# Kernel optimization log

Hardware: AMD Instinct MI355X
Metric: run time of the kernel (lower is better)

Reference implementation:

```python
import jax, jax.numpy as jnp
import numpy as np

N = 20000      # nodes
E = 320000     # edges (avg degree 16)
HID = 128      # hidden_channel
OUT = 128      # output_channel
SEQ = 8


def setup_inputs() -> dict:
    key = jax.random.key(0)
    ks = jax.random.split(key, 8)
    h = jax.random.normal(ks[0], (N, HID), jnp.float32)
    c = jax.random.normal(ks[1], (N, HID), jnp.float32)
    edge_index = jax.random.randint(ks[2], (2, E), 0, N, jnp.int64)
    edge_attr = jax.random.uniform(ks[3], (E,), jnp.float32)
    # GCNConv weights (PyG: x @ W then propagate), xavier-ish scale
    W_init = jax.random.normal(ks[4], (2 * HID, 2 * OUT), jnp.float32) * (2.0 / (2 * HID + 2 * OUT)) ** 0.5
    b_init = jnp.zeros((2 * OUT,), jnp.float32)
    W_cell = jax.random.normal(ks[5], (HID + OUT, 4 * OUT), jnp.float32) * (2.0 / (HID + OUT + 4 * OUT)) ** 0.5
    b_cell = jnp.zeros((4 * OUT,), jnp.float32)
    return {"h": h, "c": c, "edge_index": edge_index, "edge_attr": edge_attr,
            "W_init": W_init, "b_init": b_init, "W_cell": W_cell, "b_cell": b_cell,
            "seq_len": SEQ}


def _gcn(x, W, b, src, dst, ew, dinv):
    # PyG GCNConv with normalize=True, add_self_loops=True (self-loop weight 1.0)
    xw = x @ W                                   # [N, C_out]
    norm = dinv[src] * ew * dinv[dst]            # sym-normalized edge weights
    agg = jnp.zeros_like(xw).at[dst].add(xw[src] * norm[:, None])
    agg = agg + xw * (dinv * dinv)[:, None]      # self-loop term
    return agg + b


def reference(h, c, edge_index, edge_attr, W_init, b_init, W_cell, b_cell, seq_len):
    src, dst = edge_index[0], edge_index[1]
    n = h.shape[0]
    # degree with self-loops (weight 1.0), shared by both convs
    deg = jnp.zeros((n,), h.dtype).at[dst].add(edge_attr) + 1.0
    dinv = jax.lax.rsqrt(deg)

    # _init_states
    states = jax.nn.elu(_gcn(jnp.concatenate([h, c], axis=1), W_init, b_init, src, dst, edge_attr, dinv))
    h_t, c_t = states[:, :OUT], states[:, OUT:]

    def step(carry, _):
        h_cur, c_cur = carry
        # NOTE: original code feeds the initial h (not h_cur) as x each step
        combined = jnp.concatenate([h, h_cur], axis=1)
        cc = _gcn(combined, W_cell, b_cell, src, dst, edge_attr, dinv)
        cc_i, cc_f, cc_o, cc_g = jnp.split(cc, 4, axis=1)
        c_next = jax.nn.sigmoid(cc_f) * c_cur + jax.nn.sigmoid(cc_i) * jnp.tanh(cc_g)
        h_next = jax.nn.sigmoid(cc_o) * jnp.tanh(c_next)
        return (h_next, c_next), h_next

    (_, _), out = jax.lax.scan(step, (h_t, c_t), None, length=seq_len)
    return out  # [seq_len, N, OUT]
```

## Files before the change

### kernel.cpp

```cpp
#include <hip/hip_runtime.h>

#define N_NODES 20000
#define N_EDGES 320000
#define SEQ 8

typedef __attribute__((ext_vector_type(8))) short bf16x8;
typedef __attribute__((ext_vector_type(4))) float floatx4;
typedef const unsigned int __attribute__((address_space(1)))* gas_u32;
typedef unsigned int __attribute__((address_space(3)))* las_u32;

__device__ __forceinline__ unsigned short f2bf(float f) {
  unsigned int u = __builtin_bit_cast(unsigned int, f);
  return (unsigned short)((u + 0x7fffu + ((u >> 16) & 1u)) >> 16);
}
__device__ __forceinline__ float bflo(unsigned int u) {
  return __builtin_bit_cast(float, u << 16);
}
__device__ __forceinline__ float bfhi(unsigned int u) {
  return __builtin_bit_cast(float, u & 0xffff0000u);
}
__device__ __forceinline__ float sigf(float x) { return 1.f / (1.f + __expf(-x)); }

__device__ __forceinline__ void gl_lds16(const void* g, void* l) {
  auto gp = (gas_u32)g;
  auto lp = (las_u32)(unsigned int)(unsigned long long)l;
  __builtin_amdgcn_global_load_lds(gp, lp, 16, 0, 0);
}


__global__ void k_prologue(const float* __restrict__ Wi,
                           const float* __restrict__ Wc,
                           const float* __restrict__ bc,
                           unsigned short* __restrict__ WiT,
                           unsigned short* __restrict__ W1T,
                           unsigned short* __restrict__ W2T,
                           float* __restrict__ bcp,
                           float* __restrict__ deg, int* __restrict__ counts) {
  int idx = blockIdx.x * 256 + threadIdx.x;
  if (idx < N_NODES) { deg[idx] = 1.0f; counts[idx] = 0; }
  if (idx < 65536) {
    int n = idx >> 8, k = idx & 255;
    WiT[n * 256 + k] = f2bf(Wi[k * 256 + n]);
  }
  if (idx < 512) bcp[idx] = bc[((idx & 3) << 7) | (idx >> 2)];
  int n2 = idx >> 8, k2 = idx & 255;
  if (k2 < 128) {
    int orig = ((n2 & 3) << 7) | (n2 >> 2);
    W1T[n2 * 128 + k2] = f2bf(Wc[k2 * 512 + orig]);
    W2T[n2 * 128 + k2] = f2bf(Wc[(k2 + 128) * 512 + orig]);
  }
}

__global__ void k_deg(const int* __restrict__ ei, const float* __restrict__ ea,
                      float* __restrict__ deg, int* __restrict__ counts) {
  int e = blockIdx.x * 256 + threadIdx.x;
  if (e >= N_EDGES) return;
  int d = ei[N_EDGES + e];
  atomicAdd(&deg[d], ea[e]);
  atomicAdd(&counts[d], 1);
}

__global__ void k_scan1(const int* __restrict__ counts, int* __restrict__ incl,
                        int* __restrict__ part, const float* __restrict__ deg,
                        float* __restrict__ dinv) {
  __shared__ int sm[256];
  int t = threadIdx.x;
  int g = blockIdx.x * 256 + t;
  if (g < N_NODES) dinv[g] = rsqrtf(deg[g]);
  int v = (g < N_NODES) ? counts[g] : 0;
  sm[t] = v;
  __syncthreads();
  for (int o = 1; o < 256; o <<= 1) {
    int add = (t >= o) ? sm[t - o] : 0;
    __syncthreads();
    sm[t] += add;
    __syncthreads();
  }
  if (g < N_NODES) incl[g] = sm[t];
  if (t == 255) part[blockIdx.x] = sm[255];
}

__global__ void k_scan2(int* __restrict__ part, int nb) {
  __shared__ int sm[128];
  int t = threadIdx.x;
  int v = (t < nb) ? part[t] : 0;
  sm[t] = v;
  __syncthreads();
  for (int o = 1; o < 128; o <<= 1) {
    int add = (t >= o) ? sm[t - o] : 0;
    __syncthreads();
    sm[t] += add;
    __syncthreads();
  }
  if (t < nb) part[t] = sm[t] - v;
}

__global__ void k_scan3(const int* __restrict__ incl, const int* __restrict__ counts,
                        const int* __restrict__ part, int* __restrict__ row_ptr,
                        int* __restrict__ cursor) {
  int g = blockIdx.x * 256 + threadIdx.x;
  if (g < N_NODES) {
    int start = incl[g] - counts[g] + part[blockIdx.x];
    row_ptr[g] = start;
    cursor[g] = start;
  }
  if (g == 0) row_ptr[N_NODES] = N_EDGES;
}

__global__ void k_fill(const int* __restrict__ ei, const float* __restrict__ ea,
                       const float* __restrict__ dinv, int* __restrict__ cursor,
                       int* __restrict__ csr_src, float* __restrict__ csr_w) {
  int e = blockIdx.x * 256 + threadIdx.x;
  if (e >= N_EDGES) return;
  int s = ei[e], d = ei[N_EDGES + e];
  int k = atomicAdd(&cursor[d], 1);
  csr_src[k] = s;
  csr_w[k] = dinv[s] * ea[e] * dinv[d];
}


__global__ __launch_bounds__(256) void k_agg_init(
    const float* __restrict__ h, const float* __restrict__ c,
    unsigned int* __restrict__ AhAc_u, const float* __restrict__ dinv,
    const int* __restrict__ row_ptr, const int* __restrict__ csr_src,
    const float* __restrict__ csr_w) {
  int wid = (blockIdx.x * 256 + threadIdx.x) >> 6;
  int lane = threadIdx.x & 63;
  if (wid >= N_NODES) return;
  float di = dinv[wid], dd = di * di;
  const float4* xb = (lane < 32) ? (const float4*)h : (const float4*)c;
  int lcol = lane & 31;
  float4 a = xb[(size_t)wid * 32 + lcol];
  float s0 = a.x * dd, s1 = a.y * dd, s2 = a.z * dd, s3 = a.w * dd;
  int e = row_ptr[wid], end = row_ptr[wid + 1];
#pragma unroll 2
  for (; e < end; ++e) {
    int s = csr_src[e];
    float w = csr_w[e];
    float4 v = xb[(size_t)s * 32 + lcol];
    s0 += v.x * w; s1 += v.y * w; s2 += v.z * w; s3 += v.w * w;
  }
  uint2 o;
  o.x = (unsigned int)f2bf(s0) | ((unsigned int)f2bf(s1) << 16);
  o.y = (unsigned int)f2bf(s2) | ((unsigned int)f2bf(s3) << 16);
  ((uint2*)AhAc_u)[(size_t)wid * 64 + lane] = o;
}

__global__ __launch_bounds__(256) void k_agg_step(
    const unsigned int* __restrict__ hbf_u, unsigned int* __restrict__ Aht_u,
    const float* __restrict__ dinv, const int* __restrict__ row_ptr,
    const int* __restrict__ csr_src, const float* __restrict__ csr_w) {
  int wid = (blockIdx.x * 256 + threadIdx.x) >> 6;
  int lane = threadIdx.x & 63;
  if (wid >= N_NODES) return;
  float di = dinv[wid], dd = di * di;
  unsigned int a = hbf_u[(size_t)wid * 64 + lane];
  float s0 = bflo(a) * dd, s1 = bfhi(a) * dd;
  int e = row_ptr[wid], end = row_ptr[wid + 1];
#pragma unroll 2
  for (; e < end; ++e) {
    int s = csr_src[e];
    float w = csr_w[e];
    unsigned int v = hbf_u[(size_t)s * 64 + lane];
    s0 += bflo(v) * w;
    s1 += bfhi(v) * w;
  }
  Aht_u[(size_t)wid * 64 + lane] =
      (unsigned int)f2bf(s0) | ((unsigned int)f2bf(s1) << 16);
}

template <int EPI, int KK, int LDA>
__global__ __launch_bounds__(256) void k_gemm(
    const unsigned short* __restrict__ A, const unsigned short* __restrict__ BT,
    const float* __restrict__ bias, const float* __restrict__ Kbuf,
    float* __restrict__ c_cur, unsigned short* __restrict__ hbf,
    float* __restrict__ out0) {
  __shared__ __align__(16) union {
    struct { unsigned short a[128 * 64]; unsigned short b[128 * 64]; } ab;
    float ep[64 * 132];
  } sm;
  const int M = N_NODES;
  int tid = threadIdx.x;
  int bm0 = blockIdx.x * 128, bn0 = blockIdx.y * 128;
  int wave = tid >> 6, lane = tid & 63;
  int wrow = (wave >> 1) * 64, wcol = (wave & 1) * 64;
  int lr = lane & 15, lq = lane >> 4;
  int key = lr & 7;

  int lr8 = lane >> 3, cq = lane & 7;
  int gq8 = (cq ^ lr8) * 8;

  floatx4 acc[4][4];
#pragma unroll
  for (int i = 0; i < 4; i++)
#pragma unroll
    for (int j = 0; j < 4; j++) acc[i][j] = (floatx4){0.f, 0.f, 0.f, 0.f};

  for (int k0 = 0; k0 < KK; k0 += 64) {
    __syncthreads();
#pragma unroll
    for (int p = 0; p < 4; ++p) {
      int row = p * 32 + wave * 8;
      int ra = bm0 + row + lr8;
      if (ra > M - 1) ra = M - 1;
      gl_lds16(A + (size_t)ra * LDA + k0 + gq8, sm.ab.a + row * 64);
      gl_lds16(BT + (size_t)(bn0 + row + lr8) * KK + k0 + gq8,
               sm.ab.b + row * 64);
    }
    __syncthreads();
#pragma unroll
    for (int ks = 0; ks < 2; ++ks) {
      int q = ks * 4 + lq;
      int slot = (q ^ key) << 3;
      bf16x8 af[4], bfr[4];
#pragma unroll
      for (int mi = 0; mi < 4; mi++)
        af[mi] = *(const bf16x8*)(sm.ab.a + (wrow + mi * 16 + lr) * 64 + slot);
#pragma unroll
      for (int ni = 0; ni < 4; ni++)
        bfr[ni] = *(const bf16x8*)(sm.ab.b + (wcol + ni * 16 + lr) * 64 + slot);
#pragma unroll
      for (int mi = 0; mi < 4; mi++)
#pragma unroll
        for (int ni = 0; ni < 4; ni++)
          acc[mi][ni] = __builtin_amdgcn_mfma_f32_16x16x32_bf16(
              af[mi], bfr[ni], acc[mi][ni], 0, 0, 0);
    }
  }
  __syncthreads();

  if (EPI == 0) {
#pragma unroll
    for (int mi = 0; mi < 4; mi++) {
#pragma unroll
      for (int r = 0; r < 4; r++) {
        int grow = bm0 + wrow + mi * 16 + lq * 4 + r;
        if (grow >= M) continue;
#pragma unroll
        for (int ni = 0; ni < 4; ni++) {
          int gcol = bn0 + wcol + ni * 16 + lr;
          float v = acc[mi][ni][r] + bias[gcol];
          v = (v > 0.f) ? v : expm1f(v);
          if (gcol < 128) hbf[(size_t)grow * 128 + gcol] = f2bf(v);
          else c_cur[(size_t)grow * 128 + gcol - 128] = v;
        }
      }
    }
  } else if (EPI == 1) {
#pragma unroll
    for (int mi = 0; mi < 4; mi++) {
#pragma unroll
      for (int r = 0; r < 4; r++) {
        int grow = bm0 + wrow + mi * 16 + lq * 4 + r;
        if (grow >= M) continue;
#pragma unroll
        for (int ni = 0; ni < 4; ni++) {
          int gcol = bn0 + wcol + ni * 16 + lr;
          out0[(size_t)grow * 512 + gcol] = acc[mi][ni][r] + bias[gcol];
        }
      }
    }
  } else {
#pragma unroll
    for (int hch = 0; hch < 2; ++hch) {
      if ((wrow >> 6) == hch) {
#pragma unroll
        for (int mi = 0; mi < 4; mi++)
#pragma unroll
          for (int r = 0; r < 4; r++) {
            int row_l = mi * 16 + lq * 4 + r;
#pragma unroll
            for (int ni = 0; ni < 4; ni++)
              sm.ep[row_l * 132 + wcol + ni * 16 + lr] = acc[mi][ni][r];
          }
      }
      __syncthreads();
#pragma unroll
      for (int it = 0; it < 8; ++it) {
        int p = tid + it * 256;
        int row_l = p >> 5, j = p & 31;
        int grow = bm0 + hch * 64 + row_l;
        if (grow < M) {
          int jg = (bn0 >> 2) + j;
          const float* eb = sm.ep + row_l * 132 + 4 * j;
          float4 kb = *(const float4*)&Kbuf[(size_t)grow * 512 + bn0 + 4 * j];
          float gi = eb[0] + kb.x;
          float gf = eb[1] + kb.y;
          float go = eb[2] + kb.z;
          float gg = eb[3] + kb.w;
          size_t o = (size_t)grow * 128 + jg;
          float cp = c_cur[o];
          float cn = sigf(gf) * cp + sigf(gi) * tanhf(gg);
          float hn = sigf(go) * tanhf(cn);
          c_cur[o] = cn;
          hbf[o] = f2bf(hn);
          out0[o] = hn;
        }
      }
      __syncthreads();
    }
  }
}

extern "C" void kernel_launch(void* const* d_in, const int* in_sizes, int n_in,
                              void* d_out, int out_size, void* d_ws, size_t ws_size,
                              hipStream_t stream) {
  const float* h  = (const float*)d_in[0];
  const float* c  = (const float*)d_in[1];
  const int*   ei = (const int*)d_in[2];
  const float* ea = (const float*)d_in[3];
  const float* Wi = (const float*)d_in[4];
  const float* bi = (const float*)d_in[5];
  const float* Wc = (const float*)d_in[6];
  const float* bc = (const float*)d_in[7];
  float* out = (float*)d_out;

  char* w = (char*)d_ws;
  size_t off = 0;
  auto alloc = [&](size_t bytes) {
    void* p = w + off;
    off += (bytes + 511) & ~(size_t)511;
    return p;
  };
  float* deg           = (float*)alloc(N_NODES * 4);
  float* dinv          = (float*)alloc(N_NODES * 4);
  int* counts          = (int*)alloc(N_NODES * 4);
  int* cursor          = (int*)alloc(N_NODES * 4);
  int* scan_tmp        = (int*)alloc(N_NODES * 4);
  int* row_ptr         = (int*)alloc((N_NODES + 1) * 4);
  int* part            = (int*)alloc(1024 * 4);
  int* csr_src         = (int*)alloc(N_EDGES * 4);
  float* csr_w         = (float*)alloc(N_EDGES * 4);
  unsigned short* WiT  = (unsigned short*)alloc(256 * 256 * 2);
  unsigned short* W1T  = (unsigned short*)alloc(512 * 128 * 2);
  unsigned short* W2T  = (unsigned short*)alloc(512 * 128 * 2);
  float* bcp           = (float*)alloc(512 * 4);
  unsigned short* AhAc = (unsigned short*)alloc((size_t)N_NODES * 256 * 2);
  unsigned short* Aht  = (unsigned short*)alloc((size_t)N_NODES * 128 * 2);
  unsigned short* hbf  = (unsigned short*)alloc((size_t)N_NODES * 128 * 2);
  float* c_cur         = (float*)alloc((size_t)N_NODES * 128 * 4);
  float* Kbuf          = (float*)alloc((size_t)N_NODES * 512 * 4);

  const int NB_N = (N_NODES + 255) / 256;
  const int NB_E = (N_EDGES + 255) / 256;
  const int NB_AGG = N_NODES * 64 / 256;
  const int MB = (N_NODES + 127) / 128;

  k_prologue<<<512, 256, 0, stream>>>(Wi, Wc, bc, WiT, W1T, W2T, bcp, deg,
                                      counts);
  k_deg<<<NB_E, 256, 0, stream>>>(ei, ea, deg, counts);
  k_scan1<<<NB_N, 256, 0, stream>>>(counts, scan_tmp, part, deg, dinv);
  k_scan2<<<1, 128, 0, stream>>>(part, NB_N);
  k_scan3<<<NB_N, 256, 0, stream>>>(scan_tmp, counts, part, row_ptr, cursor);
  k_fill<<<NB_E, 256, 0, stream>>>(ei, ea, dinv, cursor, csr_src, csr_w);

  k_agg_init<<<NB_AGG, 256, 0, stream>>>(h, c, (unsigned int*)AhAc, dinv,
                                         row_ptr, csr_src, csr_w);
  k_gemm<0, 256, 256><<<dim3(MB, 2), 256, 0, stream>>>(
      AhAc, WiT, bi, nullptr, c_cur, hbf, nullptr);
  k_gemm<1, 128, 256><<<dim3(MB, 4), 256, 0, stream>>>(
      AhAc, W1T, bcp, nullptr, nullptr, nullptr, Kbuf);

  for (int t = 0; t < SEQ; ++t) {
    k_agg_step<<<NB_AGG, 256, 0, stream>>>((unsigned int*)hbf,
                                           (unsigned int*)Aht, dinv, row_ptr,
                                           csr_src, csr_w);
    k_gemm<2, 128, 128><<<dim3(MB, 4), 256, 0, stream>>>(
        Aht, W2T, nullptr, Kbuf, c_cur, hbf, out + (size_t)t * N_NODES * 128);
  }
}
```

Before: 567.0 us.

## Merge three-kernel prefix scan into one block and batch CSR index loads via shuffles

Replaces the three-kernel scan (block scan, partial scan, fixup) with a single 1024-thread block kernel where each thread serially scans 20 counts, removing two launches and the temporary buffers. In both aggregation kernels, each wavefront now loads up to 64 edge indices and weights cooperatively in one coalesced load and broadcasts them with shuffles, issuing four neighbor-row gathers per iteration. This aims to cut scalar-dependent latency in the edge loop and raise memory-level parallelism. The single-block scan has strided, uncoalesced accesses, and the shuffles add some per-edge cost.

New measurement: 534.7 us. 5.7% less time.

```diff
diff --git a/kernel.cpp b/kernel.cpp
--- a/kernel.cpp
+++ b/kernel.cpp
@@ -60,51 +60,42 @@
   atomicAdd(&counts[d], 1);
 }
 
-__global__ void k_scan1(const int* __restrict__ counts, int* __restrict__ incl,
-                        int* __restrict__ part, const float* __restrict__ deg,
-                        float* __restrict__ dinv) {
-  __shared__ int sm[256];
+__global__ __launch_bounds__(1024) void k_scan(
+    const int* __restrict__ counts, const float* __restrict__ deg,
+    float* __restrict__ dinv, int* __restrict__ row_ptr,
+    int* __restrict__ cursor) {
+  __shared__ int sm[1024];
   int t = threadIdx.x;
-  int g = blockIdx.x * 256 + t;
-  if (g < N_NODES) dinv[g] = rsqrtf(deg[g]);
-  int v = (g < N_NODES) ? counts[g] : 0;
-  sm[t] = v;
+  int base = t * 20;
+  int local[20];
+  int s = 0;
+#pragma unroll
+  for (int i = 0; i < 20; ++i) {
+    int g = base + i;
+    int v = (g < N_NODES) ? counts[g] : 0;
+    local[i] = v;
+    s += v;
+  }
+  sm[t] = s;
   __syncthreads();
-  for (int o = 1; o < 256; o <<= 1) {
+  for (int o = 1; o < 1024; o <<= 1) {
     int add = (t >= o) ? sm[t - o] : 0;
     __syncthreads();
     sm[t] += add;
     __syncthreads();
   }
-  if (g < N_NODES) incl[g] = sm[t];
-  if (t == 255) part[blockIdx.x] = sm[255];
-}
-
-__global__ void k_scan2(int* __restrict__ part, int nb) {
-  __shared__ int sm[128];
-  int t = threadIdx.x;
-  int v = (t < nb) ? part[t] : 0;
-  sm[t] = v;
-  __syncthreads();
-  for (int o = 1; o < 128; o <<= 1) {
-    int add = (t >= o) ? sm[t - o] : 0;
-    __syncthreads();
-    sm[t] += add;
-    __syncthreads();
-  }
-  if (t < nb) part[t] = sm[t] - v;
-}
-
-__global__ void k_scan3(const int* __restrict__ incl, const int* __restrict__ counts,
-                        const int* __restrict__ part, int* __restrict__ row_ptr,
-                        int* __restrict__ cursor) {
-  int g = blockIdx.x * 256 + threadIdx.x;
-  if (g < N_NODES) {
-    int start = incl[g] - counts[g] + part[blockIdx.x];
-    row_ptr[g] = start;
-    cursor[g] = start;
-  }
-  if (g == 0) row_ptr[N_NODES] = N_EDGES;
+  int run = sm[t] - s;
+#pragma unroll
+  for (int i = 0; i < 20; ++i) {
+    int g = base + i;
+    if (g < N_NODES) {
+      row_ptr[g] = run;
+      cursor[g] = run;
+      dinv[g] = rsqrtf(deg[g]);
+    }
+    run += local[i];
+  }
+  if (t == 0) row_ptr[N_NODES] = N_EDGES;
 }
 
 __global__ void k_fill(const int* __restrict__ ei, const float* __restrict__ ea,
@@ -132,13 +123,37 @@
   int lcol = lane & 31;
   float4 a = xb[(size_t)wid * 32 + lcol];
   float s0 = a.x * dd, s1 = a.y * dd, s2 = a.z * dd, s3 = a.w * dd;
-  int e = row_ptr[wid], end = row_ptr[wid + 1];
-#pragma unroll 2
-  for (; e < end; ++e) {
-    int s = csr_src[e];
-    float w = csr_w[e];
-    float4 v = xb[(size_t)s * 32 + lcol];
-    s0 += v.x * w; s1 += v.y * w; s2 += v.z * w; s3 += v.w * w;
+  int e0 = row_ptr[wid], end = row_ptr[wid + 1];
+  for (int base = e0; base < end; base += 64) {
+    int n = end - base;
+    if (n > 64) n = 64;
+    int sl = 0;
+    float wl = 0.f;
+    if (base + lane < end) {
+      sl = csr_src[base + lane];
+      wl = csr_w[base + lane];
+    }
+    int j = 0;
+    for (; j + 4 <= n; j += 4) {
+      int sa = __shfl(sl, j), sb = __shfl(sl, j + 1);
+      int sc = __shfl(sl, j + 2), sd = __shfl(sl, j + 3);
+      float wa = __shfl(wl, j), wb = __shfl(wl, j + 1);
+      float wc = __shfl(wl, j + 2), wd = __shfl(wl, j + 3);
+      float4 va = xb[(size_t)sa * 32 + lcol];
+      float4 vb = xb[(size_t)sb * 32 + lcol];
+      float4 vc = xb[(size_t)sc * 32 + lcol];
+      float4 vd = xb[(size_t)sd * 32 + lcol];
+      s0 += va.x * wa; s1 += va.y * wa; s2 += va.z * wa; s3 += va.w * wa;
+      s0 += vb.x * wb; s1 += vb.y * wb; s2 += vb.z * wb; s3 += vb.w * wb;
+      s0 += vc.x * wc; s1 += vc.y * wc; s2 += vc.z * wc; s3 += vc.w * wc;
+      s0 += vd.x * wd; s1 += vd.y * wd; s2 += vd.z * wd; s3 += vd.w * wd;
+    }
+    for (; j < n; ++j) {
+      int sa = __shfl(sl, j);
+      float wa = __shfl(wl, j);
+      float4 va = xb[(size_t)sa * 32 + lcol];
+      s0 += va.x * wa; s1 += va.y * wa; s2 += va.z * wa; s3 += va.w * wa;
+    }
   }
   uint2 o;
   o.x = (unsigned int)f2bf(s0) | ((unsigned int)f2bf(s1) << 16);
@@ -156,14 +171,37 @@
   float di = dinv[wid], dd = di * di;
   unsigned int a = hbf_u[(size_t)wid * 64 + lane];
   float s0 = bflo(a) * dd, s1 = bfhi(a) * dd;
-  int e = row_ptr[wid], end = row_ptr[wid + 1];
-#pragma unroll 2
-  for (; e < end; ++e) {
-    int s = csr_src[e];
-    float w = csr_w[e];
-    unsigned int v = hbf_u[(size_t)s * 64 + lane];
-    s0 += bflo(v) * w;
-    s1 += bfhi(v) * w;
+  int e0 = row_ptr[wid], end = row_ptr[wid + 1];
+  for (int base = e0; base < end; base += 64) {
+    int n = end - base;
+    if (n > 64) n = 64;
+    int sl = 0;
+    float wl = 0.f;
+    if (base + lane < end) {
+      sl = csr_src[base + lane];
+      wl = csr_w[base + lane];
+    }
+    int j = 0;
+    for (; j + 4 <= n; j += 4) {
+      int sa = __shfl(sl, j), sb = __shfl(sl, j + 1);
+      int sc = __shfl(sl, j + 2), sd = __shfl(sl, j + 3);
+      float wa = __shfl(wl, j), wb = __shfl(wl, j + 1);
+      float wc = __shfl(wl, j + 2), wd = __shfl(wl, j + 3);
+      unsigned int va = hbf_u[(size_t)sa * 64 + lane];
+      unsigned int vb = hbf_u[(size_t)sb * 64 + lane];
+      unsigned int vc = hbf_u[(size_t)sc * 64 + lane];
+      unsigned int vd = hbf_u[(size_t)sd * 64 + lane];
+      s0 += bflo(va) * wa; s1 += bfhi(va) * wa;
+      s0 += bflo(vb) * wb; s1 += bfhi(vb) * wb;
+      s0 += bflo(vc) * wc; s1 += bfhi(vc) * wc;
+      s0 += bflo(vd) * wd; s1 += bfhi(vd) * wd;
+    }
+    for (; j < n; ++j) {
+      int sa = __shfl(sl, j);
+      float wa = __shfl(wl, j);
+      unsigned int va = hbf_u[(size_t)sa * 64 + lane];
+      s0 += bflo(va) * wa; s1 += bfhi(va) * wa;
+    }
   }
   Aht_u[(size_t)wid * 64 + lane] =
       (unsigned int)f2bf(s0) | ((unsigned int)f2bf(s1) << 16);
@@ -326,9 +364,7 @@
   float* dinv          = (float*)alloc(N_NODES * 4);
   int* counts          = (int*)alloc(N_NODES * 4);
   int* cursor          = (int*)alloc(N_NODES * 4);
-  int* scan_tmp        = (int*)alloc(N_NODES * 4);
   int* row_ptr         = (int*)alloc((N_NODES + 1) * 4);
-  int* part            = (int*)alloc(1024 * 4);
   int* csr_src         = (int*)alloc(N_EDGES * 4);
   float* csr_w         = (float*)alloc(N_EDGES * 4);
   unsigned short* WiT  = (unsigned short*)alloc(256 * 256 * 2);
@@ -341,7 +377,6 @@
   float* c_cur         = (float*)alloc((size_t)N_NODES * 128 * 4);
   float* Kbuf          = (float*)alloc((size_t)N_NODES * 512 * 4);
 
-  const int NB_N = (N_NODES + 255) / 256;
   const int NB_E = (N_EDGES + 255) / 256;
   const int NB_AGG = N_NODES * 64 / 256;
   const int MB = (N_NODES + 127) / 128;
@@ -349,9 +384,7 @@
   k_prologue<<<512, 256, 0, stream>>>(Wi, Wc, bc, WiT, W1T, W2T, bcp, deg,
                                       counts);
   k_deg<<<NB_E, 256, 0, stream>>>(ei, ea, deg, counts);
-  k_scan1<<<NB_N, 256, 0, stream>>>(counts, scan_tmp, part, deg, dinv);
-  k_scan2<<<1, 128, 0, stream>>>(part, NB_N);
-  k_scan3<<<NB_N, 256, 0, stream>>>(scan_tmp, counts, part, row_ptr, cursor);
+  k_scan<<<1, 1024, 0, stream>>>(counts, deg, dinv, row_ptr, cursor);
   k_fill<<<NB_E, 256, 0, stream>>>(ei, ea, dinv, cursor, csr_src, csr_w);
 
   k_agg_init<<<NB_AGG, 256, 0, stream>>>(h, c, (unsigned int*)AhAc, dinv,
```
